# Performance work log

Hardware: AMD Instinct MI355X
Metric: run time of the kernel (lower is better)

The kernel has to match this reference:

```python
import jax, jax.numpy as jnp
import numpy as np

GROUPS = 8
EPS = 1e-5


def group_norm(x, gamma, beta):
    b, c, h, w = x.shape
    xg = x.reshape(b, GROUPS, c // GROUPS, h, w)
    mu = jnp.mean(xg, axis=(2, 3, 4), keepdims=True)
    var = jnp.mean((xg - mu) ** 2, axis=(2, 3, 4), keepdims=True)
    xn = ((xg - mu) * jax.lax.rsqrt(var + EPS)).reshape(b, c, h, w)
    return xn * gamma[None, :, None, None] + beta[None, :, None, None]


def setup_inputs() -> dict:
    key = jax.random.key(0)
    ks = jax.random.split(key, 4)
    b, c, h, w = 4, 64, 64, 64
    x = jax.random.normal(ks[0], (b, c, h, w), dtype=jnp.float32)
    gamma = jnp.ones((c,), dtype=jnp.float32)
    beta = jnp.zeros((c,), dtype=jnp.float32)
    w_qkv = jax.random.normal(ks[1], (3 * c, c), dtype=jnp.float32) * (1.0 / np.sqrt(c))
    b_qkv = jnp.zeros((3 * c,), dtype=jnp.float32)
    w_proj = jax.random.normal(ks[2], (c, c), dtype=jnp.float32) * (1.0 / np.sqrt(c))
    b_proj = jnp.zeros((c,), dtype=jnp.float32)
    return {"x": x, "gamma": gamma, "beta": beta, "w_qkv": w_qkv,
            "b_qkv": b_qkv, "w_proj": w_proj, "b_proj": b_proj}


def reference(x, gamma, beta, w_qkv, b_qkv, w_proj, b_proj):
    b, c, h, w = x.shape
    xn = group_norm(x, gamma, beta)
    # 1x1 conv == per-pixel linear: [b,3c,h,w]
    qkv = jnp.einsum('oc,bchw->bohw', w_qkv, xn) + b_qkv[None, :, None, None]
    q, k, v = jnp.split(qkv, 3, axis=1)
    # flatten spatial -> tokens: [b, hw, c]
    def tok(t):
        return t.reshape(b, c, h * w).transpose(0, 2, 1)
    q, k, v = tok(q), tok(k), tok(v)
    scale = c ** (-0.5)
    attn = jnp.einsum('bqc,bkc->bqk', q, k) * scale  # [b, hw, hw]
    attn = jax.nn.softmax(attn, axis=-1)
    out = jnp.einsum('bqk,bkc->bqc', attn, v)  # [b, hw, c]
    out = out.transpose(0, 2, 1).reshape(b, c, h, w)
    out = jnp.einsum('oc,bchw->bohw', w_proj, out) + b_proj[None, :, None, None]
    return out + x
```

## Files before the change

kernel.cpp:

```cpp
#include <hip/hip_runtime.h>

typedef __bf16 bf16x8 __attribute__((ext_vector_type(8)));
typedef __bf16 bf16x4 __attribute__((ext_vector_type(4)));
typedef float  f32x4  __attribute__((ext_vector_type(4)));
typedef float  f32x16 __attribute__((ext_vector_type(16)));

#define GLD_LDS16(gsrc, ldst) \
  __builtin_amdgcn_global_load_lds((const __attribute__((address_space(1))) void*)(gsrc), \
                                   (__attribute__((address_space(3))) void*)(ldst), 16, 0, 0)

__device__ inline unsigned cvt_pk_bf16(float lo, float hi) {
  unsigned r;
  asm("v_cvt_pk_bf16_f32 %0, %1, %2" : "=v"(r) : "v"(lo), "v"(hi));
  return r;
}
__device__ inline void pl32_swap(unsigned& a, unsigned& b) {
  asm volatile("v_permlane32_swap_b32 %0, %1" : "+v"(a), "+v"(b));
}
__device__ inline f32x16 zero16() {
  f32x16 z;
#pragma unroll
  for (int i = 0; i < 16; ++i) z[i] = 0.f;
  return z;
}

__global__ __launch_bounds__(256) void gn_partial_k(const float* __restrict__ x,
                                                    const float* __restrict__ w_qkv,
                                                    float* __restrict__ partial,
                                                    __bf16* __restrict__ whi,
                                                    __bf16* __restrict__ wlo) {
  __shared__ float red[2][4];
  const int t = threadIdx.x;
  if (blockIdx.x < 48) {
    const int idx = blockIdx.x * 256 + t;
    float wv = w_qkv[idx];
    __bf16 hh = (__bf16)wv;
    whi[idx] = hh;
    wlo[idx] = (__bf16)(wv - (float)hh);
  }
  const float4* base = (const float4*)(x + (size_t)blockIdx.x * 4096);
  float s = 0.f, sq = 0.f;
#pragma unroll
  for (int kk = 0; kk < 4; ++kk) {
    float4 v = base[t + kk * 256];
    s  += (v.x + v.y) + (v.z + v.w);
    sq += (v.x * v.x + v.y * v.y) + (v.z * v.z + v.w * v.w);
  }
#pragma unroll
  for (int o = 32; o >= 1; o >>= 1) {
    s  += __shfl_down(s, o, 64);
    sq += __shfl_down(sq, o, 64);
  }
  if ((t & 63) == 0) { red[0][t >> 6] = s; red[1][t >> 6] = sq; }
  __syncthreads();
  if (t == 0) {
    float S  = (red[0][0] + red[0][1]) + (red[0][2] + red[0][3]);
    float SQ = (red[1][0] + red[1][1]) + (red[1][2] + red[1][3]);
    partial[blockIdx.x * 2]     = S;
    partial[blockIdx.x * 2 + 1] = SQ;
  }
}

__global__ __launch_bounds__(256) void qkv_k(const float* __restrict__ x,
                                             const float* __restrict__ partial,
                                             const float* __restrict__ gamma,
                                             const float* __restrict__ beta,
                                             const __bf16* __restrict__ whi,
                                             const __bf16* __restrict__ wlo,
                                             const float* __restrict__ b_qkv,
                                             __bf16* __restrict__ qo,
                                             __bf16* __restrict__ ko,
                                             __bf16* __restrict__ vto) {
  __shared__ float mu_s[8], rs_s[8], sc_l[128];
  const int tid  = threadIdx.x;
  const int lane = tid & 63, w = tid >> 6;
  const int px16 = lane & 15, grp = lane >> 4;
  const int b    = blockIdx.x >> 6;
  const int s0   = (blockIdx.x & 63) * 64;
  const int pxg  = s0 + w * 16 + px16;

  if (tid < 8) {
    float S = 0.f, SQ = 0.f;
#pragma unroll
    for (int i = 0; i < 8; ++i) {
      S  += partial[((b * 8 + tid) * 8 + i) * 2];
      SQ += partial[((b * 8 + tid) * 8 + i) * 2 + 1];
    }
    float mean = S * (1.f / 32768.f);
    float var  = SQ * (1.f / 32768.f) - mean * mean;
    mu_s[tid] = mean;
    rs_s[tid] = rsqrtf(fmaxf(var, 0.f) + 1e-5f);
  }
  __syncthreads();
  if (tid < 64) {
    const int g = tid >> 3;
    float scale = rs_s[g] * gamma[tid];
    sc_l[tid * 2]     = scale;
    sc_l[tid * 2 + 1] = beta[tid] - mu_s[g] * scale;
  }
  __syncthreads();

  bf16x8 bh[2], bl[2];
#pragma unroll
  for (int kk = 0; kk < 2; ++kk) {
    bf16x8 hv, lv;
#pragma unroll
    for (int i = 0; i < 8; ++i) {
      const int c = kk * 32 + grp * 8 + i;
      float xv = x[((size_t)(b * 64 + c) * 4096) + pxg];
      float xn = fmaf(xv, sc_l[c * 2], sc_l[c * 2 + 1]);
      __bf16 hh = (__bf16)xn;
      hv[i] = hh;
      lv[i] = (__bf16)(xn - (float)hh);
    }
    bh[kk] = hv;
    bl[kk] = lv;
  }

  f32x4 acc[12];
#pragma unroll
  for (int ot = 0; ot < 12; ++ot) {
    const int o = ot * 16 + px16;
    f32x4 a = {0.f, 0.f, 0.f, 0.f};
#pragma unroll
    for (int kk = 0; kk < 2; ++kk) {
      const size_t wo = (size_t)o * 64 + kk * 32 + grp * 8;
      bf16x8 ah = *(const bf16x8*)(whi + wo);
      bf16x8 al = *(const bf16x8*)(wlo + wo);
      a = __builtin_amdgcn_mfma_f32_16x16x32_bf16(ah, bh[kk], a, 0, 0, 0);
      a = __builtin_amdgcn_mfma_f32_16x16x32_bf16(ah, bl[kk], a, 0, 0, 0);
      a = __builtin_amdgcn_mfma_f32_16x16x32_bf16(al, bh[kk], a, 0, 0, 0);
    }
    acc[ot] = a;
  }

#pragma unroll
  for (int ot = 0; ot < 4; ++ot) {
    const int ob = ot * 16 + grp * 4;
    float4 bias = *(const float4*)(b_qkv + ob);
    f32x4 a = acc[ot];
    bf16x4 qv = {(__bf16)((a[0] + bias.x) * 0.18033688f),
                 (__bf16)((a[1] + bias.y) * 0.18033688f),
                 (__bf16)((a[2] + bias.z) * 0.18033688f),
                 (__bf16)((a[3] + bias.w) * 0.18033688f)};
    *(bf16x4*)(qo + ((size_t)b * 4096 + pxg) * 64 + ob) = qv;
  }
#pragma unroll
  for (int ot = 4; ot < 8; ++ot) {
    const int ob = (ot - 4) * 16 + grp * 4;
    float4 bias = *(const float4*)(b_qkv + 64 + ob);
    f32x4 a = acc[ot];
    bf16x4 kv = {(__bf16)(a[0] + bias.x), (__bf16)(a[1] + bias.y),
                 (__bf16)(a[2] + bias.z), (__bf16)(a[3] + bias.w)};
    *(bf16x4*)(ko + ((size_t)b * 4096 + pxg) * 64 + ob) = kv;
  }
#pragma unroll
  for (int ot = 8; ot < 12; ++ot) {
    const int ob = (ot - 8) * 16 + grp * 4;
    float4 bias = *(const float4*)(b_qkv + 128 + ob);
    f32x4 a = acc[ot];
#pragma unroll
    for (int r = 0; r < 4; ++r) {
      float bv = (r == 0) ? bias.x : (r == 1) ? bias.y : (r == 2) ? bias.z : bias.w;
      vto[((size_t)(b * 64 + ob + r)) * 4096 + pxg] = (__bf16)(a[r] + bv);
    }
  }
}

__global__ __launch_bounds__(512, 2) void attn_k(const __bf16* __restrict__ q,
                                                 const __bf16* __restrict__ k,
                                                 const __bf16* __restrict__ vt,
                                                 __bf16* __restrict__ opart,
                                                 float* __restrict__ mlpart) {
  __shared__ __bf16 k_lds[4][4096];
  __shared__ __bf16 v_lds[4][4096];

  const int tid  = threadIdx.x;
  const int lane = tid & 63, w = tid >> 6;
  const int col  = lane & 31;
  const int h    = lane >> 5;
  const int swz  = col & 7;

  const int blk  = blockIdx.x;
  const int xcd  = blk & 7;
  const int b    = xcd >> 1;
  const int rest = blk >> 3;
  const int seg  = rest >> 3;
  const int qblk = (rest & 7) | ((xcd & 1) << 3);
  const int q0   = qblk * 256 + w * 32;
  const int j0b  = seg * 512;

  const __bf16* qp = q  + (size_t)b * 4096 * 64;
  const __bf16* kp = k  + (size_t)b * 4096 * 64;
  const __bf16* vp = vt + (size_t)b * 64 * 4096;

  bf16x8 qf[4];
#pragma unroll
  for (int kk = 0; kk < 4; ++kk)
    qf[kk] = *(const bf16x8*)(qp + (size_t)(q0 + col) * 64 + kk * 16 + h * 8);
  __builtin_amdgcn_sched_barrier(0);

  f32x16 acc0 = zero16(), acc1 = zero16();
  float m = -1e30f, l = 0.f;

  const int soff = tid * 16;
  const int sj = soff >> 7;
  const int sc2 = ((soff >> 4) & 7) ^ (sj & 7);

  auto stage = [&](int buf, int j0) {
    GLD_LDS16(kp + (size_t)(j0 + sj) * 64 + sc2 * 8, (char*)(&k_lds[buf][0]) + soff);
    GLD_LDS16(vp + (size_t)sj * 4096 + j0 + sc2 * 8, (char*)(&v_lds[buf][0]) + soff);
  };

  stage(0, j0b);
  stage(1, j0b + 64);
  stage(2, j0b + 128);
  stage(3, j0b + 192);

#pragma unroll
  for (int kt = 0; kt < 4; ++kt) {
    if (kt == 0) asm volatile("s_waitcnt vmcnt(4)" ::: "memory");
    else         asm volatile("s_waitcnt vmcnt(0)" ::: "memory");
    __builtin_amdgcn_s_barrier();

    if (kt == 1) { stage(0, j0b + 256); stage(1, j0b + 320); }
    if (kt == 2) { stage(2, j0b + 384); stage(3, j0b + 448); }

#pragma unroll
    for (int sub = 0; sub < 2; ++sub) {
      const int buf = (2 * kt + sub) & 3;
      const char* kbase = (const char*)&k_lds[buf][0];
      const char* vbase = (const char*)&v_lds[buf][0];

      f32x16 sa0 = zero16(), sa1 = zero16();
      __builtin_amdgcn_s_setprio(1);
#pragma unroll
      for (int kk = 0; kk < 4; ++kk) {
        bf16x8 kf0 = *(const bf16x8*)(kbase + col * 128        + (((2 * kk + h) ^ swz) << 4));
        bf16x8 kf1 = *(const bf16x8*)(kbase + (32 + col) * 128 + (((2 * kk + h) ^ swz) << 4));
        sa0 = __builtin_amdgcn_mfma_f32_32x32x16_bf16(kf0, qf[kk], sa0, 0, 0, 0);
        sa1 = __builtin_amdgcn_mfma_f32_32x32x16_bf16(kf1, qf[kk], sa1, 0, 0, 0);
      }
      __builtin_amdgcn_s_setprio(0);

      float x0 = fmaxf(fmaxf(sa0[0], sa0[1]),   fmaxf(sa0[2], sa0[3]));
      float x1 = fmaxf(fmaxf(sa0[4], sa0[5]),   fmaxf(sa0[6], sa0[7]));
      float x2 = fmaxf(fmaxf(sa0[8], sa0[9]),   fmaxf(sa0[10], sa0[11]));
      float x3 = fmaxf(fmaxf(sa0[12], sa0[13]), fmaxf(sa0[14], sa0[15]));
      float y0 = fmaxf(fmaxf(sa1[0], sa1[1]),   fmaxf(sa1[2], sa1[3]));
      float y1 = fmaxf(fmaxf(sa1[4], sa1[5]),   fmaxf(sa1[6], sa1[7]));
      float y2 = fmaxf(fmaxf(sa1[8], sa1[9]),   fmaxf(sa1[10], sa1[11]));
      float y3 = fmaxf(fmaxf(sa1[12], sa1[13]), fmaxf(sa1[14], sa1[15]));
      float mx = fmaxf(fmaxf(fmaxf(x0, x1), fmaxf(x2, x3)),
                       fmaxf(fmaxf(y0, y1), fmaxf(y2, y3)));
      mx = fmaxf(mx, __shfl_xor(mx, 32, 64));
      if (!__all(mx <= m + 8.f)) {
        float mn = fmaxf(m, mx);
        float sf = exp2f(m - mn);
        m = mn;
        l *= sf;
        acc0 *= sf;
        acc1 *= sf;
      }
      float ls = 0.f;
#pragma unroll
      for (int r = 0; r < 16; ++r) { sa0[r] = exp2f(sa0[r] - m); ls += sa0[r]; }
#pragma unroll
      for (int r = 0; r < 16; ++r) { sa1[r] = exp2f(sa1[r] - m); ls += sa1[r]; }
      l += ls;

      unsigned w0[8], w1[8];
#pragma unroll
      for (int qd = 0; qd < 4; ++qd) {
        w0[qd * 2]     = cvt_pk_bf16(sa0[4 * qd],     sa0[4 * qd + 1]);
        w0[qd * 2 + 1] = cvt_pk_bf16(sa0[4 * qd + 2], sa0[4 * qd + 3]);
        w1[qd * 2]     = cvt_pk_bf16(sa1[4 * qd],     sa1[4 * qd + 1]);
        w1[qd * 2 + 1] = cvt_pk_bf16(sa1[4 * qd + 2], sa1[4 * qd + 3]);
      }
      bf16x8 pa[4];
#pragma unroll
      for (int c = 0; c < 4; ++c) {
        const unsigned* wt = (c < 2) ? w0 : w1;
        unsigned a0 = wt[(2 * (c & 1)) * 2],     b0 = wt[(2 * (c & 1) + 1) * 2];
        unsigned a1 = wt[(2 * (c & 1)) * 2 + 1], b1 = wt[(2 * (c & 1) + 1) * 2 + 1];
        pl32_swap(a0, b0);
        pl32_swap(a1, b1);
        uint4 u; u.x = a0; u.y = a1; u.z = b0; u.w = b1;
        pa[c] = __builtin_bit_cast(bf16x8, u);
      }

      __builtin_amdgcn_s_setprio(1);
#pragma unroll
      for (int c = 0; c < 4; ++c) {
        bf16x8 vf0 = *(const bf16x8*)(vbase + col * 128        + (((2 * c + h) ^ swz) << 4));
        bf16x8 vf1 = *(const bf16x8*)(vbase + (32 + col) * 128 + (((2 * c + h) ^ swz) << 4));
        acc0 = __builtin_amdgcn_mfma_f32_32x32x16_bf16(vf0, pa[c], acc0, 0, 0, 0);
        acc1 = __builtin_amdgcn_mfma_f32_32x32x16_bf16(vf1, pa[c], acc1, 0, 0, 0);
      }
      __builtin_amdgcn_s_setprio(0);
    }
  }

  float lf = l + __shfl_xor(l, 32, 64);
  const int qrow = q0 + col;
  __bf16* ob = opart + ((size_t)(b * 8 + seg) * 4096 + qrow) * 64;
#pragma unroll
  for (int rq = 0; rq < 4; ++rq) {
    const int d0 = 8 * rq + 4 * h;
    bf16x4 o0 = {(__bf16)acc0[4 * rq], (__bf16)acc0[4 * rq + 1],
                 (__bf16)acc0[4 * rq + 2], (__bf16)acc0[4 * rq + 3]};
    bf16x4 o1 = {(__bf16)acc1[4 * rq], (__bf16)acc1[4 * rq + 1],
                 (__bf16)acc1[4 * rq + 2], (__bf16)acc1[4 * rq + 3]};
    *(bf16x4*)(ob + d0)      = o0;
    *(bf16x4*)(ob + 32 + d0) = o1;
  }
  if (h == 0) {
    float2 mlv; mlv.x = m; mlv.y = lf;
    *(float2*)(mlpart + ((size_t)(b * 8 + seg) * 4096 + qrow) * 2) = mlv;
  }
}

__global__ __launch_bounds__(256) void proj_k(const __bf16* __restrict__ opart,
                                              const float* __restrict__ mlpart,
                                              const float* __restrict__ x,
                                              const float* __restrict__ w_proj,
                                              const float* __restrict__ b_proj,
                                              float* __restrict__ out) {
  __shared__ float wseg[8][32];
  __shared__ float a_lds[32 * 68];
  __shared__ float o_lds[64 * 33];
  const int t  = threadIdx.x;
  const int b  = blockIdx.x >> 7;
  const int s0 = (blockIdx.x & 127) * 32;

  if (t < 32) {
    const int rowg = s0 + t;
    float ms[8], ls[8], es[8];
    float M = -1e30f;
#pragma unroll
    for (int s = 0; s < 8; ++s) {
      float2 ml = *(const float2*)(mlpart + ((size_t)(b * 8 + s) * 4096 + rowg) * 2);
      ms[s] = ml.x; ls[s] = ml.y;
      M = fmaxf(M, ms[s]);
    }
    float L = 0.f;
#pragma unroll
    for (int s = 0; s < 8; ++s) { es[s] = exp2f(ms[s] - M); L += es[s] * ls[s]; }
    float invL = 1.f / L;
#pragma unroll
    for (int s = 0; s < 8; ++s) wseg[s][t] = es[s] * invL;
  }
  __syncthreads();

  for (int i = t; i < 512; i += 256) {
    const int px = i >> 4, c4 = i & 15;
    const __bf16* obase = opart + ((size_t)(b * 8) * 4096 + s0 + px) * 64 + c4 * 4;
    float4 a = {0.f, 0.f, 0.f, 0.f};
#pragma unroll
    for (int s = 0; s < 8; ++s) {
      bf16x4 v = *(const bf16x4*)(obase + (size_t)s * 4096 * 64);
      float wv = wseg[s][px];
      a.x += wv * (float)v[0]; a.y += wv * (float)v[1];
      a.z += wv * (float)v[2]; a.w += wv * (float)v[3];
    }
    *(float4*)(&a_lds[px * 68 + c4 * 4]) = a;
  }

  const int o = t & 63, wg = t >> 6;
  float4 wr[16];
  const float4* wrow = (const float4*)(w_proj + o * 64);
#pragma unroll
  for (int i = 0; i < 16; ++i) wr[i] = wrow[i];
  const float bias = b_proj[o];
  __syncthreads();

  for (int pp = 0; pp < 8; ++pp) {
    const int px = wg * 8 + pp;
    const float4* ar = (const float4*)&a_lds[px * 68];
    float a0 = bias, a1 = 0.f, a2 = 0.f, a3 = 0.f;
#pragma unroll
    for (int i = 0; i < 16; i += 4) {
      float4 x0 = ar[i], x1 = ar[i + 1], x2 = ar[i + 2], x3 = ar[i + 3];
      a0 += wr[i    ].x * x0.x + wr[i    ].y * x0.y + wr[i    ].z * x0.z + wr[i    ].w * x0.w;
      a1 += wr[i + 1].x * x1.x + wr[i + 1].y * x1.y + wr[i + 1].z * x1.z + wr[i + 1].w * x1.w;
      a2 += wr[i + 2].x * x2.x + wr[i + 2].y * x2.y + wr[i + 2].z * x2.z + wr[i + 2].w * x2.w;
      a3 += wr[i + 3].x * x3.x + wr[i + 3].y * x3.y + wr[i + 3].z * x3.z + wr[i + 3].w * x3.w;
    }
    o_lds[o * 33 + px] = (a0 + a1) + (a2 + a3);
  }
  __syncthreads();
  for (int idx = t; idx < 2048; idx += 256) {
    const int c = idx >> 5, px = idx & 31;
    const size_t gi = ((size_t)(b * 64 + c)) * 4096 + s0 + px;
    out[gi] = o_lds[c * 33 + px] + x[gi];
  }
}

extern "C" void kernel_launch(void* const* d_in, const int* in_sizes, int n_in,
                              void* d_out, int out_size, void* d_ws, size_t ws_size,
                              hipStream_t stream) {
  const float* x      = (const float*)d_in[0];
  const float* gamma  = (const float*)d_in[1];
  const float* beta   = (const float*)d_in[2];
  const float* w_qkv  = (const float*)d_in[3];
  const float* b_qkv  = (const float*)d_in[4];
  const float* w_proj = (const float*)d_in[5];
  const float* b_proj = (const float*)d_in[6];
  float* out = (float*)d_out;

  char* ws = (char*)d_ws;
  float*  partial = (float*)ws;
  __bf16* whi     = (__bf16*)(ws + 4096);
  __bf16* wlo     = whi + 12288;
  __bf16* qb  = (__bf16*)(ws + 65536);
  __bf16* kb  = qb  + (size_t)4 * 4096 * 64;
  __bf16* vtb = kb  + (size_t)4 * 4096 * 64;
  __bf16* opart = vtb + (size_t)4 * 4096 * 64;
  float*  mlpart = (float*)(opart + (size_t)4 * 8 * 4096 * 64);

  gn_partial_k<<<256, 256, 0, stream>>>(x, w_qkv, partial, whi, wlo);
  qkv_k<<<256, 256, 0, stream>>>(x, partial, gamma, beta, whi, wlo, b_qkv, qb, kb, vtb);
  attn_k<<<512, 512, 0, stream>>>(qb, kb, vtb, opart, mlpart);
  proj_k<<<512, 256, 0, stream>>>(opart, mlpart, x, w_proj, b_proj, out);
}
```

Measured before the change: 67.81 us.

## Drop LDS staging in attention; load K/V fragments directly from global

Removes the async global-to-LDS multi-buffered staging of K and V tiles, so each wave now reads its MFMA operand fragments straight from global memory, relying on L1/L2 caching. Blocks shrink from 512 to 256 threads with 128 queries each, and the grid doubles to 1024 to keep the same coverage. This drops the barriers, LDS footprint and waitcnt choreography, but every wave re-fetches the same K/V tiles through the cache, which raises global load traffic and exposes load latency without an explicit prefetch pipeline.

```diff
diff --git a/kernel.cpp b/kernel.cpp
--- a/kernel.cpp
+++ b/kernel.cpp
@@ -4,10 +4,6 @@
 typedef __bf16 bf16x4 __attribute__((ext_vector_type(4)));
 typedef float  f32x4  __attribute__((ext_vector_type(4)));
 typedef float  f32x16 __attribute__((ext_vector_type(16)));
-
-#define GLD_LDS16(gsrc, ldst) \
-  __builtin_amdgcn_global_load_lds((const __attribute__((address_space(1))) void*)(gsrc), \
-                                   (__attribute__((address_space(3))) void*)(ldst), 16, 0, 0)
 
 __device__ inline unsigned cvt_pk_bf16(float lo, float hi) {
   unsigned r;
@@ -167,27 +163,23 @@
   }
 }
 
-__global__ __launch_bounds__(512, 2) void attn_k(const __bf16* __restrict__ q,
+__global__ __launch_bounds__(256, 4) void attn_k(const __bf16* __restrict__ q,
                                                  const __bf16* __restrict__ k,
                                                  const __bf16* __restrict__ vt,
                                                  __bf16* __restrict__ opart,
                                                  float* __restrict__ mlpart) {
-  __shared__ __bf16 k_lds[4][4096];
-  __shared__ __bf16 v_lds[4][4096];
-
   const int tid  = threadIdx.x;
   const int lane = tid & 63, w = tid >> 6;
   const int col  = lane & 31;
   const int h    = lane >> 5;
-  const int swz  = col & 7;
 
   const int blk  = blockIdx.x;
   const int xcd  = blk & 7;
   const int b    = xcd >> 1;
   const int rest = blk >> 3;
-  const int seg  = rest >> 3;
-  const int qblk = (rest & 7) | ((xcd & 1) << 3);
-  const int q0   = qblk * 256 + w * 32;
+  const int seg  = rest >> 4;
+  const int qblk = (rest & 15) | ((xcd & 1) << 4);
+  const int q0   = qblk * 128 + w * 32;
   const int j0b  = seg * 512;
 
   const __bf16* qp = q  + (size_t)b * 4096 * 64;
@@ -198,107 +190,85 @@
 #pragma unroll
   for (int kk = 0; kk < 4; ++kk)
     qf[kk] = *(const bf16x8*)(qp + (size_t)(q0 + col) * 64 + kk * 16 + h * 8);
-  __builtin_amdgcn_sched_barrier(0);
 
   f32x16 acc0 = zero16(), acc1 = zero16();
   float m = -1e30f, l = 0.f;
 
-  const int soff = tid * 16;
-  const int sj = soff >> 7;
-  const int sc2 = ((soff >> 4) & 7) ^ (sj & 7);
-
-  auto stage = [&](int buf, int j0) {
-    GLD_LDS16(kp + (size_t)(j0 + sj) * 64 + sc2 * 8, (char*)(&k_lds[buf][0]) + soff);
-    GLD_LDS16(vp + (size_t)sj * 4096 + j0 + sc2 * 8, (char*)(&v_lds[buf][0]) + soff);
-  };
-
-  stage(0, j0b);
-  stage(1, j0b + 64);
-  stage(2, j0b + 128);
-  stage(3, j0b + 192);
-
-#pragma unroll
-  for (int kt = 0; kt < 4; ++kt) {
-    if (kt == 0) asm volatile("s_waitcnt vmcnt(4)" ::: "memory");
-    else         asm volatile("s_waitcnt vmcnt(0)" ::: "memory");
-    __builtin_amdgcn_s_barrier();
-
-    if (kt == 1) { stage(0, j0b + 256); stage(1, j0b + 320); }
-    if (kt == 2) { stage(2, j0b + 384); stage(3, j0b + 448); }
-
-#pragma unroll
-    for (int sub = 0; sub < 2; ++sub) {
-      const int buf = (2 * kt + sub) & 3;
-      const char* kbase = (const char*)&k_lds[buf][0];
-      const char* vbase = (const char*)&v_lds[buf][0];
-
-      f32x16 sa0 = zero16(), sa1 = zero16();
-      __builtin_amdgcn_s_setprio(1);
-#pragma unroll
-      for (int kk = 0; kk < 4; ++kk) {
-        bf16x8 kf0 = *(const bf16x8*)(kbase + col * 128        + (((2 * kk + h) ^ swz) << 4));
-        bf16x8 kf1 = *(const bf16x8*)(kbase + (32 + col) * 128 + (((2 * kk + h) ^ swz) << 4));
-        sa0 = __builtin_amdgcn_mfma_f32_32x32x16_bf16(kf0, qf[kk], sa0, 0, 0, 0);
-        sa1 = __builtin_amdgcn_mfma_f32_32x32x16_bf16(kf1, qf[kk], sa1, 0, 0, 0);
-      }
-      __builtin_amdgcn_s_setprio(0);
-
-      float x0 = fmaxf(fmaxf(sa0[0], sa0[1]),   fmaxf(sa0[2], sa0[3]));
-      float x1 = fmaxf(fmaxf(sa0[4], sa0[5]),   fmaxf(sa0[6], sa0[7]));
-      float x2 = fmaxf(fmaxf(sa0[8], sa0[9]),   fmaxf(sa0[10], sa0[11]));
-      float x3 = fmaxf(fmaxf(sa0[12], sa0[13]), fmaxf(sa0[14], sa0[15]));
-      float y0 = fmaxf(fmaxf(sa1[0], sa1[1]),   fmaxf(sa1[2], sa1[3]));
-      float y1 = fmaxf(fmaxf(sa1[4], sa1[5]),   fmaxf(sa1[6], sa1[7]));
-      float y2 = fmaxf(fmaxf(sa1[8], sa1[9]),   fmaxf(sa1[10], sa1[11]));
-      float y3 = fmaxf(fmaxf(sa1[12], sa1[13]), fmaxf(sa1[14], sa1[15]));
-      float mx = fmaxf(fmaxf(fmaxf(x0, x1), fmaxf(x2, x3)),
-                       fmaxf(fmaxf(y0, y1), fmaxf(y2, y3)));
-      mx = fmaxf(mx, __shfl_xor(mx, 32, 64));
-      if (!__all(mx <= m + 8.f)) {
-        float mn = fmaxf(m, mx);
-        float sf = exp2f(m - mn);
-        m = mn;
-        l *= sf;
-        acc0 *= sf;
-        acc1 *= sf;
-      }
-      float ls = 0.f;
-#pragma unroll
-      for (int r = 0; r < 16; ++r) { sa0[r] = exp2f(sa0[r] - m); ls += sa0[r]; }
-#pragma unroll
-      for (int r = 0; r < 16; ++r) { sa1[r] = exp2f(sa1[r] - m); ls += sa1[r]; }
-      l += ls;
-
-      unsigned w0[8], w1[8];
-#pragma unroll
-      for (int qd = 0; qd < 4; ++qd) {
-        w0[qd * 2]     = cvt_pk_bf16(sa0[4 * qd],     sa0[4 * qd + 1]);
-        w0[qd * 2 + 1] = cvt_pk_bf16(sa0[4 * qd + 2], sa0[4 * qd + 3]);
-        w1[qd * 2]     = cvt_pk_bf16(sa1[4 * qd],     sa1[4 * qd + 1]);
-        w1[qd * 2 + 1] = cvt_pk_bf16(sa1[4 * qd + 2], sa1[4 * qd + 3]);
-      }
-      bf16x8 pa[4];
-#pragma unroll
-      for (int c = 0; c < 4; ++c) {
-        const unsigned* wt = (c < 2) ? w0 : w1;
-        unsigned a0 = wt[(2 * (c & 1)) * 2],     b0 = wt[(2 * (c & 1) + 1) * 2];
-        unsigned a1 = wt[(2 * (c & 1)) * 2 + 1], b1 = wt[(2 * (c & 1) + 1) * 2 + 1];
-        pl32_swap(a0, b0);
-        pl32_swap(a1, b1);
-        uint4 u; u.x = a0; u.y = a1; u.z = b0; u.w = b1;
-        pa[c] = __builtin_bit_cast(bf16x8, u);
-      }
-
-      __builtin_amdgcn_s_setprio(1);
-#pragma unroll
-      for (int c = 0; c < 4; ++c) {
-        bf16x8 vf0 = *(const bf16x8*)(vbase + col * 128        + (((2 * c + h) ^ swz) << 4));
-        bf16x8 vf1 = *(const bf16x8*)(vbase + (32 + col) * 128 + (((2 * c + h) ^ swz) << 4));
-        acc0 = __builtin_amdgcn_mfma_f32_32x32x16_bf16(vf0, pa[c], acc0, 0, 0, 0);
-        acc1 = __builtin_amdgcn_mfma_f32_32x32x16_bf16(vf1, pa[c], acc1, 0, 0, 0);
-      }
-      __builtin_amdgcn_s_setprio(0);
-    }
+  const __bf16* krow0 = kp + (size_t)col * 64;
+  const __bf16* krow1 = kp + (size_t)(32 + col) * 64;
+  const __bf16* vrow0 = vp + (size_t)col * 4096;
+  const __bf16* vrow1 = vp + (size_t)(32 + col) * 4096;
+
+#pragma unroll
+  for (int kt = 0; kt < 8; ++kt) {
+    const int j0 = j0b + kt * 64;
+
+    f32x16 sa0 = zero16(), sa1 = zero16();
+    __builtin_amdgcn_s_setprio(1);
+#pragma unroll
+    for (int kk = 0; kk < 4; ++kk) {
+      bf16x8 kf0 = *(const bf16x8*)(krow0 + (size_t)j0 * 64 + kk * 16 + h * 8);
+      bf16x8 kf1 = *(const bf16x8*)(krow1 + (size_t)j0 * 64 + kk * 16 + h * 8);
+      sa0 = __builtin_amdgcn_mfma_f32_32x32x16_bf16(kf0, qf[kk], sa0, 0, 0, 0);
+      sa1 = __builtin_amdgcn_mfma_f32_32x32x16_bf16(kf1, qf[kk], sa1, 0, 0, 0);
+    }
+    __builtin_amdgcn_s_setprio(0);
+
+    float x0 = fmaxf(fmaxf(sa0[0], sa0[1]),   fmaxf(sa0[2], sa0[3]));
+    float x1 = fmaxf(fmaxf(sa0[4], sa0[5]),   fmaxf(sa0[6], sa0[7]));
+    float x2 = fmaxf(fmaxf(sa0[8], sa0[9]),   fmaxf(sa0[10], sa0[11]));
+    float x3 = fmaxf(fmaxf(sa0[12], sa0[13]), fmaxf(sa0[14], sa0[15]));
+    float y0 = fmaxf(fmaxf(sa1[0], sa1[1]),   fmaxf(sa1[2], sa1[3]));
+    float y1 = fmaxf(fmaxf(sa1[4], sa1[5]),   fmaxf(sa1[6], sa1[7]));
+    float y2 = fmaxf(fmaxf(sa1[8], sa1[9]),   fmaxf(sa1[10], sa1[11]));
+    float y3 = fmaxf(fmaxf(sa1[12], sa1[13]), fmaxf(sa1[14], sa1[15]));
+    float mx = fmaxf(fmaxf(fmaxf(x0, x1), fmaxf(x2, x3)),
+                     fmaxf(fmaxf(y0, y1), fmaxf(y2, y3)));
+    mx = fmaxf(mx, __shfl_xor(mx, 32, 64));
+    if (!__all(mx <= m + 8.f)) {
+      float mn = fmaxf(m, mx);
+      float sf = exp2f(m - mn);
+      m = mn;
+      l *= sf;
+      acc0 *= sf;
+      acc1 *= sf;
+    }
+    float ls = 0.f;
+#pragma unroll
+    for (int r = 0; r < 16; ++r) { sa0[r] = exp2f(sa0[r] - m); ls += sa0[r]; }
+#pragma unroll
+    for (int r = 0; r < 16; ++r) { sa1[r] = exp2f(sa1[r] - m); ls += sa1[r]; }
+    l += ls;
+
+    unsigned w0[8], w1[8];
+#pragma unroll
+    for (int qd = 0; qd < 4; ++qd) {
+      w0[qd * 2]     = cvt_pk_bf16(sa0[4 * qd],     sa0[4 * qd + 1]);
+      w0[qd * 2 + 1] = cvt_pk_bf16(sa0[4 * qd + 2], sa0[4 * qd + 3]);
+      w1[qd * 2]     = cvt_pk_bf16(sa1[4 * qd],     sa1[4 * qd + 1]);
+      w1[qd * 2 + 1] = cvt_pk_bf16(sa1[4 * qd + 2], sa1[4 * qd + 3]);
+    }
+    bf16x8 pa[4];
+#pragma unroll
+    for (int c = 0; c < 4; ++c) {
+      const unsigned* wt = (c < 2) ? w0 : w1;
+      unsigned a0 = wt[(2 * (c & 1)) * 2],     b0 = wt[(2 * (c & 1) + 1) * 2];
+      unsigned a1 = wt[(2 * (c & 1)) * 2 + 1], b1 = wt[(2 * (c & 1) + 1) * 2 + 1];
+      pl32_swap(a0, b0);
+      pl32_swap(a1, b1);
+      uint4 u; u.x = a0; u.y = a1; u.z = b0; u.w = b1;
+      pa[c] = __builtin_bit_cast(bf16x8, u);
+    }
+
+    __builtin_amdgcn_s_setprio(1);
+#pragma unroll
+    for (int c = 0; c < 4; ++c) {
+      bf16x8 vf0 = *(const bf16x8*)(vrow0 + j0 + c * 16 + h * 8);
+      bf16x8 vf1 = *(const bf16x8*)(vrow1 + j0 + c * 16 + h * 8);
+      acc0 = __builtin_amdgcn_mfma_f32_32x32x16_bf16(vf0, pa[c], acc0, 0, 0, 0);
+      acc1 = __builtin_amdgcn_mfma_f32_32x32x16_bf16(vf1, pa[c], acc1, 0, 0, 0);
+    }
+    __builtin_amdgcn_s_setprio(0);
   }
 
   float lf = l + __shfl_xor(l, 32, 64);
@@ -420,6 +390,6 @@
 
   gn_partial_k<<<256, 256, 0, stream>>>(x, w_qkv, partial, whi, wlo);
   qkv_k<<<256, 256, 0, stream>>>(x, partial, gamma, beta, whi, wlo, b_qkv, qb, kb, vtb);
-  attn_k<<<512, 512, 0, stream>>>(qb, kb, vtb, opart, mlpart);
+  attn_k<<<1024, 256, 0, stream>>>(qb, kb, vtb, opart, mlpart);
   proj_k<<<512, 256, 0, stream>>>(opart, mlpart, x, w_proj, b_proj, out);
 }
```

Measured after the change: 101.0 us. +49.0%, slower.
